# Kernel tuning notes

Hardware: AMD Instinct MI355X
Metric: run time of the kernel (lower is better)

The kernel has to match this reference:

```python
import jax, jax.numpy as jnp
import numpy as np

B, N = 128, 4096
D_WHAT = 64
NEG_FRAC = 0.1
EPS = 1e-3


def setup_inputs() -> dict:
    rng = np.random.RandomState(0)
    # per-row present counts, deterministic, max = 256 -> static n_objects
    counts = 200 + (np.arange(B) % 57)  # max = 200 + 56 = 256
    max_present = int(counts.max())
    n_objects = max_present + int(NEG_FRAC * N)  # 256 + 409 = 665
    # random present positions per row: rank of a random matrix
    prio = rng.rand(B, N)
    rank = np.argsort(np.argsort(prio, axis=1), axis=1)
    present = (rank < counts[:, None]).astype(np.float32)  # [B, N]
    z_present = jnp.asarray(present[..., None])  # [B, N, 1], values in {0, 1}

    key = jax.random.key(0)
    k = jax.random.split(key, 6)
    return {
        "z_where": jax.random.uniform(k[0], (B, N, 4), dtype=jnp.float32),
        "z_present": z_present,
        "z_what_loc": jax.random.normal(k[1], (B, N, D_WHAT), dtype=jnp.float32),
        "z_what_scale": jax.random.uniform(k[2], (B, N, D_WHAT), dtype=jnp.float32) + 0.1,
        "z_depth_loc": jax.random.normal(k[3], (B, N, 1), dtype=jnp.float32),
        "z_depth_scale": jax.random.uniform(k[4], (B, N, 1), dtype=jnp.float32) + 0.1,
        "neg_priority": jax.random.uniform(k[5], (B, N), dtype=jnp.float32),
        "n_objects": n_objects,
    }


def reference(z_where, z_present, z_what_loc, z_what_scale,
              z_depth_loc, z_depth_scale, neg_priority, n_objects):
    # --- reset_non_present: latents with z_present <= eps get (loc=0, scale=1) ---
    mask = z_present > EPS  # [B, N, 1], broadcasts over feature dim
    z_what_loc = jnp.where(mask, z_what_loc, 0.0)
    z_what_scale = jnp.where(mask, z_what_scale, 1.0)
    z_depth_loc = jnp.where(mask, z_depth_loc, 0.0)
    z_depth_scale = jnp.where(mask, z_depth_scale, 1.0)

    # --- convert_to_square: wh -> max(w, h) for both dims ---
    wh_idx = jnp.argmax(z_where[..., 2:], axis=-1) + 2  # [B, N]
    m = jnp.take_along_axis(z_where, wh_idx[..., None], axis=-1)  # [B, N, 1]
    z_where_sq = jnp.concatenate([z_where[..., :2], m, m], axis=-1)  # [B, N, 4]

    # representation fns: where_fn/present_fn = identity, what_fn/depth_fn = loc
    zp = z_present  # [B, N, 1]

    # --- add_negative: mark (n_objects - n_present) random absent slots with -1 ---
    n_present = jnp.sum(zp[..., 0], axis=1).astype(jnp.int32)  # [B]
    zero_mask = zp[..., 0] == 0  # [B, N]
    prio = jnp.where(zero_mask, neg_priority, jnp.inf)
    rank = jnp.argsort(jnp.argsort(prio, axis=1), axis=1)  # per-row rank of priorities
    n_neg = n_objects - n_present  # [B]
    neg_mask = zero_mask & (rank < n_neg[:, None])  # [B, N]
    modified = jnp.where(neg_mask[..., None], -1.0, zp)  # [B, N, 1]

    # --- filter_representation: keep slots with modified != 0, exactly n_objects/row ---
    present_mask = modified[..., 0] != 0  # [B, N], exactly n_objects True per row
    # stable argsort on ~mask puts True slots first, preserving original order
    idx = jnp.argsort(~present_mask, axis=1, stable=True)[:, :n_objects]  # [B, K]
    gather = lambda t: jnp.take_along_axis(t, idx[..., None], axis=1)

    return (gather(z_where_sq),   # [B, K, 4]
            gather(modified),     # [B, K, 1]
            gather(z_what_loc),   # [B, K, 64]
            gather(z_depth_loc))  # [B, K, 1]
```

## Files before the change

### kernel.cpp

```cpp
#include <hip/hip_runtime.h>
#include <stdint.h>

typedef unsigned int   u32;
typedef unsigned long long u64;

#define Bb   128
#define Nn   4096
#define DW   64
#define TPB  256
#define PERT 16
#define NBINS 4096
#define LCAP 512
#define CCAP 1024
#define BPR  8

__device__ __forceinline__ int wave_iscan(int v) {
    int lane = threadIdx.x & 63;
    #pragma unroll
    for (int d = 1; d < 64; d <<= 1) {
        int u = __shfl_up(v, d, 64);
        v += (lane >= d) ? u : 0;
    }
    return v;
}

__device__ __forceinline__ int block_escan(int v, int* wsum) {
    int tid  = threadIdx.x;
    int wid  = tid >> 6;
    int incl = wave_iscan(v);
    if ((tid & 63) == 63) wsum[wid] = incl;
    __syncthreads();
    int base = 0;
    #pragma unroll
    for (int w = 0; w < TPB / 64; w++) base += (w < wid) ? wsum[w] : 0;
    return base + incl - v;
}

template<bool DO_COPY>
__global__ __launch_bounds__(TPB) void sel_kernel(
    const float* __restrict__ zwhere, const float* __restrict__ zpres,
    const float* __restrict__ zwhat,  const float* __restrict__ zdepth,
    const float* __restrict__ nprio,
    float* __restrict__ out0, float* __restrict__ out1,
    float* __restrict__ out2, float* __restrict__ out3,
    int* __restrict__ srcws, int K)
{
    __shared__ u32 hist[NBINS];
    __shared__ u64 blist[LCAP];
    __shared__ int compact[CCAP];
    __shared__ int wsumA[4], wsumB[4];
    __shared__ int s_m, s_bstar, s_cbefore, s_np;
    __shared__ u64 s_thr;

    const int b   = blockIdx.x;
    const int tid = threadIdx.x;

    for (int i = tid; i < NBINS; i += TPB) hist[i] = 0;
    if (tid == 0) { s_m = 0; s_bstar = -1; s_cbefore = 0; s_np = 0; s_thr = 0; }

    float p[PERT];
    u32 pm = 0;
    {
        const float4* zp4 = (const float4*)(zpres + (size_t)b * Nn);
        const float4* pr4 = (const float4*)(nprio + (size_t)b * Nn);
        #pragma unroll
        for (int q = 0; q < 4; q++) {
            float4 z  = zp4[tid * 4 + q];
            float4 pp = pr4[tid * 4 + q];
            p[4*q+0] = pp.x; p[4*q+1] = pp.y; p[4*q+2] = pp.z; p[4*q+3] = pp.w;
            if (z.x != 0.0f) pm |= 1u << (4*q+0);
            if (z.y != 0.0f) pm |= 1u << (4*q+1);
            if (z.z != 0.0f) pm |= 1u << (4*q+2);
            if (z.w != 0.0f) pm |= 1u << (4*q+3);
        }
    }
    __syncthreads();

    #pragma unroll
    for (int j = 0; j < PERT; j++) {
        if (!((pm >> j) & 1u)) {
            int bin = (int)(p[j] * (float)NBINS);
            bin = bin < 0 ? 0 : (bin > NBINS - 1 ? NBINS - 1 : bin);
            atomicAdd(&hist[bin], 1u);
        }
    }
    {
        int myp = __popc(pm);
        #pragma unroll
        for (int d = 32; d >= 1; d >>= 1) myp += __shfl_down(myp, d, 64);
        if ((tid & 63) == 0) atomicAdd(&s_np, myp);
    }
    __syncthreads();

    const int n_neg = K - s_np;

    int hl = 0;
    #pragma unroll
    for (int j = 0; j < 16; j++) hl += (int)hist[tid * 16 + j];
    int hbase = block_escan(hl, wsumA);
    if (n_neg > hbase && n_neg <= hbase + hl) {
        int c = hbase;
        for (int j = 0; j < 16; j++) {
            int h = (int)hist[tid * 16 + j];
            if (n_neg <= c + h) { s_bstar = tid * 16 + j; s_cbefore = c; break; }
            c += h;
        }
    }
    __syncthreads();
    const int bstar = s_bstar;
    const int r     = n_neg - s_cbefore;

    #pragma unroll
    for (int j = 0; j < PERT; j++) {
        if (!((pm >> j) & 1u)) {
            int bin = (int)(p[j] * (float)NBINS);
            bin = bin < 0 ? 0 : (bin > NBINS - 1 ? NBINS - 1 : bin);
            if (bin == bstar) {
                int pos = atomicAdd(&s_m, 1);
                if (pos < LCAP)
                    blist[pos] = (((u64)__float_as_uint(p[j])) << 12) | (u64)(tid * PERT + j);
            }
        }
    }
    __syncthreads();
    {
        int m = s_m; if (m > LCAP) m = LCAP;
        for (int j2 = tid; j2 < m; j2 += TPB) {
            u64 kj = blist[j2];
            int rank = 0;
            for (int l = 0; l < m; l++) rank += (blist[l] < kj) ? 1 : 0;
            if (rank == r - 1) s_thr = kj;
        }
    }
    __syncthreads();
    const u64 thr = s_thr;

    u32 selbits = 0, negbits = 0;
    int lc = 0;
    #pragma unroll
    for (int j = 0; j < PERT; j++) {
        bool present = (pm >> j) & 1u;
        bool neg = false;
        if (!present) {
            int bin = (int)(p[j] * (float)NBINS);
            bin = bin < 0 ? 0 : (bin > NBINS - 1 ? NBINS - 1 : bin);
            u64 key = (((u64)__float_as_uint(p[j])) << 12) | (u64)(tid * PERT + j);
            neg = (bin < bstar) || (bin == bstar && key <= thr);
        }
        if (present || neg) { selbits |= 1u << j; lc++; }
        if (neg) negbits |= 1u << j;
    }
    int pos = block_escan(lc, wsumB);
    #pragma unroll
    for (int j = 0; j < PERT; j++) {
        if ((selbits >> j) & 1u) {
            if (pos < CCAP)
                compact[pos] = (tid * PERT + j) | ((((negbits >> j) & 1u)) << 30);
            pos++;
        }
    }
    __syncthreads();

    if (!DO_COPY) {
        for (int k = tid; k < K; k += TPB)
            srcws[(size_t)b * K + k] = compact[k];
        return;
    }

    for (int i = tid; i < K * 16; i += TPB) {
        int k = i >> 4, lane = i & 15;
        int e = compact[k];
        int src = e & (Nn - 1);
        bool neg = (e >> 30) & 1;
        float4 v = make_float4(0.f, 0.f, 0.f, 0.f);
        if (!neg) v = *(const float4*)(zwhat + ((size_t)(b * Nn + src) * DW + lane * 4));
        *(float4*)(out2 + ((size_t)(b * K + k) * DW + lane * 4)) = v;
    }
    for (int k = tid; k < K; k += TPB) {
        int e = compact[k];
        int src = e & (Nn - 1);
        bool neg = (e >> 30) & 1;
        float4 w = *(const float4*)(zwhere + (size_t)(b * Nn + src) * 4);
        float mv = (w.z >= w.w) ? w.z : w.w;
        float4 o; o.x = w.x; o.y = w.y; o.z = mv; o.w = mv;
        *(float4*)(out0 + (size_t)(b * K + k) * 4) = o;
        out1[(size_t)b * K + k] = neg ? -1.0f : 1.0f;
        out3[(size_t)b * K + k] = neg ? 0.0f : zdepth[(size_t)b * Nn + src];
    }
}

__global__ __launch_bounds__(TPB) void copy_kernel(
    const float* __restrict__ zwhere, const float* __restrict__ zwhat,
    const float* __restrict__ zdepth, const int* __restrict__ srcws,
    float* __restrict__ out0, float* __restrict__ out1,
    float* __restrict__ out2, float* __restrict__ out3,
    int K, int spb)
{
    int b     = blockIdx.x / BPR;
    int chunk = blockIdx.x % BPR;
    int k0 = chunk * spb;
    int k1 = k0 + spb; if (k1 > K) k1 = K;
    int tid = threadIdx.x;

    for (int i = k0 * 16 + tid; i < k1 * 16; i += TPB) {
        int k = i >> 4, lane = i & 15;
        int e = srcws[(size_t)b * K + k];
        int src = e & (Nn - 1);
        bool neg = (e >> 30) & 1;
        float4 v = make_float4(0.f, 0.f, 0.f, 0.f);
        if (!neg) v = *(const float4*)(zwhat + ((size_t)(b * Nn + src) * DW + lane * 4));
        *(float4*)(out2 + ((size_t)(b * K + k) * DW + lane * 4)) = v;
    }
    for (int k = k0 + tid; k < k1; k += TPB) {
        int e = srcws[(size_t)b * K + k];
        int src = e & (Nn - 1);
        bool neg = (e >> 30) & 1;
        float4 w = *(const float4*)(zwhere + (size_t)(b * Nn + src) * 4);
        float mv = (w.z >= w.w) ? w.z : w.w;
        float4 o; o.x = w.x; o.y = w.y; o.z = mv; o.w = mv;
        *(float4*)(out0 + (size_t)(b * K + k) * 4) = o;
        out1[(size_t)b * K + k] = neg ? -1.0f : 1.0f;
        out3[(size_t)b * K + k] = neg ? 0.0f : zdepth[(size_t)b * Nn + src];
    }
}

extern "C" void kernel_launch(void* const* d_in, const int* in_sizes, int n_in,
                              void* d_out, int out_size, void* d_ws, size_t ws_size,
                              hipStream_t stream) {
    const float* zwhere = (const float*)d_in[0];
    const float* zpres  = (const float*)d_in[1];
    const float* zwhat  = (const float*)d_in[2];
    const float* zdepth = (const float*)d_in[4];
    const float* nprio  = (const float*)d_in[6];
    int K = out_size / (Bb * 70);

    float* out  = (float*)d_out;
    float* out0 = out;
    float* out1 = out0 + (size_t)Bb * K * 4;
    float* out2 = out1 + (size_t)Bb * K;
    float* out3 = out2 + (size_t)Bb * K * DW;

    size_t need = (size_t)Bb * K * sizeof(int);
    if (ws_size >= need) {
        int* srcws = (int*)d_ws;
        sel_kernel<false><<<Bb, TPB, 0, stream>>>(zwhere, zpres, zwhat, zdepth, nprio,
                                                  out0, out1, out2, out3, srcws, K);
        int spb = (K + BPR - 1) / BPR;
        copy_kernel<<<Bb * BPR, TPB, 0, stream>>>(zwhere, zwhat, zdepth, srcws,
                                                  out0, out1, out2, out3, K, spb);
    } else {
        sel_kernel<true><<<Bb, TPB, 0, stream>>>(zwhere, zpres, zwhat, zdepth, nprio,
                                                 out0, out1, out2, out3, nullptr, K);
    }
}
```

Before: 253.2 us.

## Fuse selection and gather into one kernel with redundant per-chunk selection

Merges the selection kernel and the copy kernel into a single launch of B*8 blocks. Each block recomputes the full per-row selection (histogram, threshold, compaction) and then gathers only its slice of output slots. This removes the second launch and the workspace round-trip for source indices, at the cost of doing the selection work eight times per row.

```diff
diff --git a/kernel.cpp b/kernel.cpp
--- a/kernel.cpp
+++ b/kernel.cpp
@@ -36,14 +36,13 @@
     return base + incl - v;
 }
 
-template<bool DO_COPY>
-__global__ __launch_bounds__(TPB) void sel_kernel(
+__global__ __launch_bounds__(TPB) void fused_kernel(
     const float* __restrict__ zwhere, const float* __restrict__ zpres,
     const float* __restrict__ zwhat,  const float* __restrict__ zdepth,
     const float* __restrict__ nprio,
     float* __restrict__ out0, float* __restrict__ out1,
     float* __restrict__ out2, float* __restrict__ out3,
-    int* __restrict__ srcws, int K)
+    int K, int spb)
 {
     __shared__ u32 hist[NBINS];
     __shared__ u64 blist[LCAP];
@@ -52,8 +51,9 @@
     __shared__ int s_m, s_bstar, s_cbefore, s_np;
     __shared__ u64 s_thr;
 
-    const int b   = blockIdx.x;
-    const int tid = threadIdx.x;
+    const int b     = blockIdx.x / BPR;
+    const int chunk = blockIdx.x % BPR;
+    const int tid   = threadIdx.x;
 
     for (int i = tid; i < NBINS; i += TPB) hist[i] = 0;
     if (tid == 0) { s_m = 0; s_bstar = -1; s_cbefore = 0; s_np = 0; s_thr = 0; }
@@ -161,13 +161,10 @@
     }
     __syncthreads();
 
-    if (!DO_COPY) {
-        for (int k = tid; k < K; k += TPB)
-            srcws[(size_t)b * K + k] = compact[k];
-        return;
-    }
-
-    for (int i = tid; i < K * 16; i += TPB) {
+    const int k0 = chunk * spb;
+    int k1 = k0 + spb; if (k1 > K) k1 = K;
+
+    for (int i = k0 * 16 + tid; i < k1 * 16; i += TPB) {
         int k = i >> 4, lane = i & 15;
         int e = compact[k];
         int src = e & (Nn - 1);
@@ -176,7 +173,7 @@
         if (!neg) v = *(const float4*)(zwhat + ((size_t)(b * Nn + src) * DW + lane * 4));
         *(float4*)(out2 + ((size_t)(b * K + k) * DW + lane * 4)) = v;
     }
-    for (int k = tid; k < K; k += TPB) {
+    for (int k = k0 + tid; k < k1; k += TPB) {
         int e = compact[k];
         int src = e & (Nn - 1);
         bool neg = (e >> 30) & 1;
@@ -189,41 +186,6 @@
     }
 }
 
-__global__ __launch_bounds__(TPB) void copy_kernel(
-    const float* __restrict__ zwhere, const float* __restrict__ zwhat,
-    const float* __restrict__ zdepth, const int* __restrict__ srcws,
-    float* __restrict__ out0, float* __restrict__ out1,
-    float* __restrict__ out2, float* __restrict__ out3,
-    int K, int spb)
-{
-    int b     = blockIdx.x / BPR;
-    int chunk = blockIdx.x % BPR;
-    int k0 = chunk * spb;
-    int k1 = k0 + spb; if (k1 > K) k1 = K;
-    int tid = threadIdx.x;
-
-    for (int i = k0 * 16 + tid; i < k1 * 16; i += TPB) {
-        int k = i >> 4, lane = i & 15;
-        int e = srcws[(size_t)b * K + k];
-        int src = e & (Nn - 1);
-        bool neg = (e >> 30) & 1;
-        float4 v = make_float4(0.f, 0.f, 0.f, 0.f);
-        if (!neg) v = *(const float4*)(zwhat + ((size_t)(b * Nn + src) * DW + lane * 4));
-        *(float4*)(out2 + ((size_t)(b * K + k) * DW + lane * 4)) = v;
-    }
-    for (int k = k0 + tid; k < k1; k += TPB) {
-        int e = srcws[(size_t)b * K + k];
-        int src = e & (Nn - 1);
-        bool neg = (e >> 30) & 1;
-        float4 w = *(const float4*)(zwhere + (size_t)(b * Nn + src) * 4);
-        float mv = (w.z >= w.w) ? w.z : w.w;
-        float4 o; o.x = w.x; o.y = w.y; o.z = mv; o.w = mv;
-        *(float4*)(out0 + (size_t)(b * K + k) * 4) = o;
-        out1[(size_t)b * K + k] = neg ? -1.0f : 1.0f;
-        out3[(size_t)b * K + k] = neg ? 0.0f : zdepth[(size_t)b * Nn + src];
-    }
-}
-
 extern "C" void kernel_launch(void* const* d_in, const int* in_sizes, int n_in,
                               void* d_out, int out_size, void* d_ws, size_t ws_size,
                               hipStream_t stream) {
@@ -240,16 +202,8 @@
     float* out2 = out1 + (size_t)Bb * K;
     float* out3 = out2 + (size_t)Bb * K * DW;
 
-    size_t need = (size_t)Bb * K * sizeof(int);
-    if (ws_size >= need) {
-        int* srcws = (int*)d_ws;
-        sel_kernel<false><<<Bb, TPB, 0, stream>>>(zwhere, zpres, zwhat, zdepth, nprio,
-                                                  out0, out1, out2, out3, srcws, K);
-        int spb = (K + BPR - 1) / BPR;
-        copy_kernel<<<Bb * BPR, TPB, 0, stream>>>(zwhere, zwhat, zdepth, srcws,
-                                                  out0, out1, out2, out3, K, spb);
-    } else {
-        sel_kernel<true><<<Bb, TPB, 0, stream>>>(zwhere, zpres, zwhat, zdepth, nprio,
-                                                 out0, out1, out2, out3, nullptr, K);
-    }
-}
+    int spb = (K + BPR - 1) / BPR;
+    fused_kernel<<<Bb * BPR, TPB, 0, stream>>>(zwhere, zpres, zwhat, zdepth, nprio,
+                                               out0, out1, out2, out3, K, spb);
+    (void)d_ws; (void)ws_size;
+}
```

Result: no change. 252.3 us (-0.4%).
